# Optimization experiments

Measured on AMD Instinct MI355X. Metric: run time of the kernel, lower is better.

## Reference

```python
import jax, jax.numpy as jnp
import numpy as np

B, T, C = 4, 2048, 1024
N_HEADS = 16
HEAD_DIM = C // N_HEADS


def setup_inputs() -> dict:
    key = jax.random.key(0)
    k1, k2, k3, k4, k5 = jax.random.split(key, 5)
    x = jax.random.normal(k1, (B, T, C), dtype=jnp.float32)
    # torch Linear: y = x @ W.T + b; store W as [out, in]
    w_qkv = jax.random.normal(k2, (3 * C, C), dtype=jnp.float32) * (1.0 / np.sqrt(C))
    b_qkv = jax.random.normal(k3, (3 * C,), dtype=jnp.float32) * 0.01
    w_proj = jax.random.normal(k4, (C, C), dtype=jnp.float32) * (1.0 / np.sqrt(C))
    b_proj = jax.random.normal(k5, (C,), dtype=jnp.float32) * 0.01
    return {"x": x, "w_qkv": w_qkv, "b_qkv": b_qkv, "w_proj": w_proj, "b_proj": b_proj}


def reference(x, w_qkv, b_qkv, w_proj, b_proj):
    Bx, Tx, Cx = x.shape
    scale = 1.0 / np.sqrt(HEAD_DIM)
    qkv = x @ w_qkv.T + b_qkv                              # [B,T,3C]
    qkv = qkv.reshape(Bx, Tx, 3, N_HEADS, HEAD_DIM)
    qkv = jnp.transpose(qkv, (2, 0, 3, 1, 4))              # [3,B,H,T,D]
    q, k, v = qkv[0], qkv[1], qkv[2]
    att = jnp.einsum('bhqd,bhkd->bhqk', q, k) * scale      # [B,H,T,T]
    causal = jnp.tril(jnp.ones((Tx, Tx), dtype=bool))
    att = jnp.where(causal[None, None, :, :], att, -jnp.inf)
    att = jax.nn.softmax(att, axis=-1)
    # dropout p=0.0 (eval) -> identity
    out = jnp.einsum('bhqk,bhkd->bhqd', att, v)            # [B,H,T,D]
    out = jnp.transpose(out, (0, 2, 1, 3)).reshape(Bx, Tx, Cx)
    return out @ w_proj.T + b_proj
```

## Files before the change

kernel.cpp:

```cpp
#include <hip/hip_runtime.h>
#include <hip/hip_bf16.h>
#include <cstdint>

typedef __attribute__((ext_vector_type(8))) short bf16x8;
typedef __attribute__((ext_vector_type(4))) float f32x4;
typedef __attribute__((ext_vector_type(16))) float f32x16;

#define MFMA16(a, b, c) __builtin_amdgcn_mfma_f32_16x16x32_bf16(a, b, c, 0, 0, 0)
#define MFMA32(a, b, c) __builtin_amdgcn_mfma_f32_32x32x16_bf16(a, b, c, 0, 0, 0)

typedef __attribute__((address_space(1))) uint32_t as1_u32;
typedef __attribute__((address_space(3))) uint32_t as3_u32;
static __device__ __forceinline__ void gload16(const void* g, void* l) {
  __builtin_amdgcn_global_load_lds((as1_u32*)g, (as3_u32*)l, 16, 0, 0);
}

static __device__ __forceinline__ ushort f2b(float f) {
  union { float f; uint32_t u; } v; v.f = f;
  uint32_t u = v.u;
  uint32_t r = (u + 0x7FFFu + ((u >> 16) & 1u)) >> 16;
  return (ushort)r;
}

static __device__ __forceinline__ uint32_t cvtpk(float a, float b) {
  uint32_t r;
  asm("v_cvt_pk_bf16_f32 %0, %1, %2" : "=v"(r) : "v"(a), "v"(b));
  return r;
}
static __device__ __forceinline__ void plswap(uint32_t& a, uint32_t& b) {
  asm volatile("v_permlane32_swap_b32 %0, %1" : "+v"(a), "+v"(b));
}

#define QSCALE 0.1803368782f

#define LOFF(r, kc4) (((r) >> 1) * 64 + ((((((r) & 1) << 2) | (kc4)) ^ (((r) >> 1) & 7)) * 8))

#define N4_X  2097152
#define N4_WQ 786432
#define N4_WP 262144
__global__ void cvt_all(const float* __restrict__ x, const float* __restrict__ wq,
                        const float* __restrict__ wp, ushort* __restrict__ xb,
                        ushort* __restrict__ wqb, ushort* __restrict__ wpb) {
  int i = blockIdx.x * blockDim.x + threadIdx.x;
  const float* src; ushort* dst; int j;
  if (i < N4_X)            { src = x;  dst = xb;  j = i; }
  else if (i < N4_X + N4_WQ) { src = wq; dst = wqb; j = i - N4_X; }
  else                     { src = wp; dst = wpb; j = i - (N4_X + N4_WQ); }
  const float4 v = ((const float4*)src)[j];
  ushort4 o;
  o.x = f2b(v.x); o.y = f2b(v.y); o.z = f2b(v.z); o.w = f2b(v.w);
  ((ushort4*)dst)[j] = o;
}

template<int EPI>
__global__ __launch_bounds__(512, 2) void gemm_2ph(
    const ushort* __restrict__ A,
    const ushort* __restrict__ W,
    const float* __restrict__ bias,
    int M, int N, int K,
    ushort* __restrict__ q_ws, ushort* __restrict__ k_ws, ushort* __restrict__ v_ws,
    float* __restrict__ out) {
  __shared__ ushort As[2][2][64 * 64];
  __shared__ ushort Bs[2][2][2][64 * 64];
  const int tid = threadIdx.x;
  const int nbx = N >> 8;
  const int cpx = gridDim.x >> 3;
  const int wg = (blockIdx.x & 7) * cpx + (blockIdx.x >> 3);
  const int m0 = (wg / nbx) * 128, n0 = (wg % nbx) * 256;
  const int wid = tid >> 6, lane = tid & 63;
  const int wr = wid >> 2, wc = wid & 3;
  const int lr = lane & 15, lg = lane >> 4;
  const int prow = tid >> 3, pchk = tid & 7;
  const int lchk = pchk ^ (prow & 7);
  const int srow = prow * 2 + (lchk >> 2);
  const int skc = (lchk & 3) * 8;

  f32x4 acc[4][4] = {};
  const int nt = K >> 6;

#define STA(db_, kt_)                                                         \
  { const ushort* src = A + (size_t)(m0 + srow) * K + (kt_)*64 + skc;         \
    gload16(src, &As[db_][0][tid * 8]);                                       \
    gload16(src + 32, &As[db_][1][tid * 8]); }
#define STB(db_, half_, kt_)                                                  \
  { const ushort* src = W + (size_t)(n0 + (half_)*128 + srow) * K + (kt_)*64 + skc; \
    gload16(src, &Bs[db_][half_][0][tid * 8]);                                \
    gload16(src + 32, &Bs[db_][half_][1][tid * 8]); }

  STB(0, 0, 0); STB(0, 1, 0);
  STA(0, 0);
  STB(1, 0, 1); STB(1, 1, 1);
  asm volatile("s_waitcnt vmcnt(4)" ::: "memory");
  __builtin_amdgcn_s_barrier();

  const int bhalf = wc >> 1, brow = (wc & 1) * 64;
  for (int T = 0; T < nt; ++T) {
    const int db = T & 1;
    const ushort* Asub0 = &As[db][0][0];
    const ushort* Asub1 = &As[db][1][0];
    const ushort* Bsub0 = &Bs[db][bhalf][0][0];
    const ushort* Bsub1 = &Bs[db][bhalf][1][0];
    bf16x8 b[4][2];
    {
      bf16x8 a[2][2];
#pragma unroll
      for (int mm = 0; mm < 2; ++mm) {
        const int r = wr * 64 + mm * 16 + lr;
        a[mm][0] = *(const bf16x8*)&Asub0[LOFF(r, lg)];
        a[mm][1] = *(const bf16x8*)&Asub1[LOFF(r, lg)];
      }
#pragma unroll
      for (int nf = 0; nf < 4; ++nf) {
        const int r = brow + nf * 16 + lr;
        b[nf][0] = *(const bf16x8*)&Bsub0[LOFF(r, lg)];
        b[nf][1] = *(const bf16x8*)&Bsub1[LOFF(r, lg)];
      }
      if (T + 1 < nt) STA((T + 1) & 1, T + 1);
      __builtin_amdgcn_sched_barrier(0);
      __builtin_amdgcn_s_barrier();
      asm volatile("s_waitcnt lgkmcnt(0)" ::: "memory");
      __builtin_amdgcn_sched_barrier(0);
      __builtin_amdgcn_s_setprio(1);
#pragma unroll
      for (int kk = 0; kk < 2; ++kk)
#pragma unroll
        for (int mm = 0; mm < 2; ++mm)
#pragma unroll
          for (int nf = 0; nf < 4; ++nf)
            acc[mm][nf] = MFMA16(a[mm][kk], b[nf][kk], acc[mm][nf]);
      __builtin_amdgcn_s_setprio(0);
      __builtin_amdgcn_s_barrier();
    }
    {
      bf16x8 a[2][2];
#pragma unroll
      for (int mm = 0; mm < 2; ++mm) {
        const int r = wr * 64 + (2 + mm) * 16 + lr;
        a[mm][0] = *(const bf16x8*)&Asub0[LOFF(r, lg)];
        a[mm][1] = *(const bf16x8*)&Asub1[LOFF(r, lg)];
      }
      if (T + 2 < nt) { STB(db, 0, T + 2); STB(db, 1, T + 2); }
      __builtin_amdgcn_sched_barrier(0);
      __builtin_amdgcn_s_barrier();
      asm volatile("s_waitcnt lgkmcnt(0)" ::: "memory");
      __builtin_amdgcn_sched_barrier(0);
      __builtin_amdgcn_s_setprio(1);
#pragma unroll
      for (int kk = 0; kk < 2; ++kk)
#pragma unroll
        for (int mm = 0; mm < 2; ++mm)
#pragma unroll
          for (int nf = 0; nf < 4; ++nf)
            acc[2 + mm][nf] = MFMA16(a[mm][kk], b[nf][kk], acc[2 + mm][nf]);
      __builtin_amdgcn_s_setprio(0);
      if (T + 2 < nt)
        asm volatile("s_waitcnt vmcnt(4)" ::: "memory");
      else if (T + 1 < nt)
        asm volatile("s_waitcnt vmcnt(0)" ::: "memory");
      if (T + 1 < nt) __builtin_amdgcn_s_barrier();
    }
  }
#undef STA
#undef STB

#pragma unroll
  for (int mf = 0; mf < 4; ++mf) {
#pragma unroll
    for (int nf = 0; nf < 4; ++nf) {
      const int rowb = m0 + wr * 64 + mf * 16 + lg * 4;
      const int col = n0 + wc * 64 + nf * 16 + lr;
      float v[4];
#pragma unroll
      for (int i = 0; i < 4; ++i) v[i] = acc[mf][nf][i] + bias[col];
      if (EPI == 0) {
        const int sel = col >> 10;
        const int rem = col & 1023;
        const int h = rem >> 6, d = rem & 63;
        const int bb = rowb >> 11, t0 = rowb & 2047;
        if (sel == 2) {
          ushort4 st;
          st.x = f2b(v[0]); st.y = f2b(v[1]); st.z = f2b(v[2]); st.w = f2b(v[3]);
          *(ushort4*)&v_ws[((size_t)(bb * 16 + h) * 64 + d) * 2048 + t0] = st;
        } else if (sel == 0) {
#pragma unroll
          for (int i = 0; i < 4; ++i)
            q_ws[((size_t)(bb * 16 + h) * 2048 + t0 + i) * 64 + d] = f2b(v[i] * QSCALE);
        } else {
#pragma unroll
          for (int i = 0; i < 4; ++i)
            k_ws[((size_t)(bb * 16 + h) * 2048 + t0 + i) * 64 + d] = f2b(v[i]);
        }
      } else {
#pragma unroll
        for (int i = 0; i < 4; ++i)
          out[(size_t)(rowb + i) * N + col] = v[i];
      }
    }
  }
}

__global__ __launch_bounds__(256, 4) void attn_v6(
    const ushort* __restrict__ Q, const ushort* __restrict__ K,
    const ushort* __restrict__ VT, ushort* __restrict__ O ) {
  const int blk = blockIdx.x;
  const int s = 15 - (blk >> 6);
  const int bh = blk & 63;
  const int tid = threadIdx.x;
  const int w = tid >> 6, lane = tid & 63;
  const int l31 = lane & 31, l5 = lane >> 5;
  const int bb = bh >> 4, h = bh & 15;
  const size_t base = (size_t)bh * 2048 * 64;
  const ushort* Qb = Q + base;
  const ushort* Kb = K + base;
  const ushort* VTb = VT + base;

  __shared__ ushort Ks[2][64 * 64];
  __shared__ ushort Vs[2][64 * 64];
  __shared__ float l_lds[4][32];

#define STAGE(buf, kt_)                                              \
  do {                                                               \
    const ushort* Kt = Kb + (size_t)(kt_) * 64 * 64;                 \
    const ushort* Vt = VTb + (kt_) * 64;                             \
    _Pragma("unroll") for (int i_ = 0; i_ < 2; ++i_) {               \
      const int ch = i_ * 256 + tid;                                 \
      const int r = ch >> 3;                                         \
      const int csw = ((ch & 7) ^ (r & 7)) * 8;                      \
      gload16(&Kt[(size_t)r * 64 + csw], &Ks[buf][ch * 8]);          \
      gload16(&Vt[(size_t)r * 2048 + csw], &Vs[buf][ch * 8]);        \
    }                                                                \
  } while (0)

  const int q0w = s * 128 + w * 32;
  const int nt = 2 * s + 2;
  const int qlane = q0w + l31;

  bf16x8 qf[4];
#pragma unroll
  for (int dblk = 0; dblk < 4; ++dblk)
    qf[dblk] = *(const bf16x8*)&Qb[(size_t)qlane * 64 + dblk * 16 + l5 * 8];

  f32x16 o0 = {}, o1 = {};
  float lsum = 0.f;

  STAGE(0, 0);
  __syncthreads();

  for (int kt = 0; kt < nt; ++kt) {
    const int cur = kt & 1;
    if (kt + 1 < nt) STAGE(cur ^ 1, kt + 1);
    const int k0 = kt << 6;
    const ushort* Ksc = Ks[cur];
    const ushort* Vsc = Vs[cur];
#pragma unroll
    for (int kblk = 0; kblk < 2; ++kblk) {
      const int kbase = k0 + kblk * 32;
      if (kbase <= q0w + 31) {
        f32x16 st = {};
        __builtin_amdgcn_s_setprio(1);
#pragma unroll
        for (int dblk = 0; dblk < 4; ++dblk) {
          const int row = kblk * 32 + l31;
          bf16x8 ka = *(const bf16x8*)&Ksc[row * 64 + (((dblk * 2 + l5) ^ (row & 7)) * 8)];
          st = MFMA32(ka, qf[dblk], st);
        }
        __builtin_amdgcn_s_setprio(0);
        if (kbase + 31 > q0w) {
#pragma unroll
          for (int r = 0; r < 16; ++r) {
            const int kk = kbase + (r & 3) + 8 * (r >> 2) + 4 * l5;
            st[r] = (kk <= qlane) ? st[r] : -INFINITY;
          }
        }
        float p[16];
#pragma unroll
        for (int r = 0; r < 16; ++r) {
          p[r] = __builtin_amdgcn_exp2f(st[r]);
          lsum += p[r];
        }
#pragma unroll
        for (int sbl = 0; sbl < 2; ++sbl) {
          uint32_t P0 = cvtpk(p[8 * sbl + 0], p[8 * sbl + 1]);
          uint32_t P1 = cvtpk(p[8 * sbl + 2], p[8 * sbl + 3]);
          uint32_t P2 = cvtpk(p[8 * sbl + 4], p[8 * sbl + 5]);
          uint32_t P3 = cvtpk(p[8 * sbl + 6], p[8 * sbl + 7]);
          plswap(P0, P2);
          plswap(P1, P3);
          union { uint32_t u[4]; bf16x8 v; } pk;
          pk.u[0] = P0; pk.u[1] = P1; pk.u[2] = P2; pk.u[3] = P3;
          const int kchunk = kblk * 4 + sbl * 2 + l5;
          __builtin_amdgcn_s_setprio(1);
#pragma unroll
          for (int db2 = 0; db2 < 2; ++db2) {
            const int vrow = db2 * 32 + l31;
            bf16x8 vb = *(const bf16x8*)&Vsc[vrow * 64 + ((kchunk ^ (vrow & 7)) * 8)];
            if (db2 == 0) o0 = MFMA32(pk.v, vb, o0);
            else          o1 = MFMA32(pk.v, vb, o1);
          }
          __builtin_amdgcn_s_setprio(0);
        }
      }
    }
    __syncthreads();
  }

  const float lfull = lsum + __shfl_xor(lsum, 32);
  if (lane < 32) l_lds[w][lane] = 1.f / lfull;
#pragma unroll
  for (int r = 0; r < 16; ++r) {
    const int qoff = (r & 3) + 8 * (r >> 2) + 4 * l5;
    const float inv = l_lds[w][qoff];
    const int t = q0w + qoff;
    ushort* op = &O[(size_t)(bb * 2048 + t) * 1024 + h * 64 + l31];
    op[0] = f2b(o0[r] * inv);
    op[32] = f2b(o1[r] * inv);
  }
#undef STAGE
}

extern "C" void kernel_launch(void* const* d_in, const int* in_sizes, int n_in,
                              void* d_out, int out_size, void* d_ws, size_t ws_size,
                              hipStream_t stream) {
  const float* x = (const float*)d_in[0];
  const float* w_qkv = (const float*)d_in[1];
  const float* b_qkv = (const float*)d_in[2];
  const float* w_proj = (const float*)d_in[3];
  const float* b_proj = (const float*)d_in[4];
  float* out = (float*)d_out;

  char* ws = (char*)d_ws;
  const size_t SZ_X = (size_t)8192 * 1024 * 2;
  const size_t SZ_WQ = (size_t)3072 * 1024 * 2;
  const size_t SZ_WP = (size_t)1024 * 1024 * 2;
  ushort* xb = (ushort*)(ws);
  ushort* wqb = (ushort*)(ws + SZ_X);
  ushort* wpb = (ushort*)(ws + SZ_X + SZ_WQ);
  ushort* q_ws = (ushort*)(ws + SZ_X + SZ_WQ + SZ_WP);
  ushort* k_ws = q_ws + (size_t)8192 * 1024;
  ushort* v_ws = k_ws + (size_t)8192 * 1024;

  cvt_all<<<(N4_X + N4_WQ + N4_WP) / 256, 256, 0, stream>>>(
      x, w_qkv, w_proj, xb, wqb, wpb);

  gemm_2ph<0><<<768, 512, 0, stream>>>(
      xb, wqb, b_qkv, 8192, 3072, 1024, q_ws, k_ws, v_ws, nullptr);

  attn_v6<<<1024, 256, 0, stream>>>(q_ws, k_ws, v_ws, xb);

  gemm_2ph<1><<<256, 512, 0, stream>>>(
      xb, wpb, b_proj, 8192, 1024, 1024, nullptr, nullptr, nullptr, out);
}
```

Before: 156.7 us.

## Use 256x256 tiles for QKV GEMM with split A-phase pipeline

```diff
diff --git a/kernel.cpp b/kernel.cpp
--- a/kernel.cpp
+++ b/kernel.cpp
@@ -52,13 +52,149 @@
   ((ushort4*)dst)[j] = o;
 }
 
-template<int EPI>
-__global__ __launch_bounds__(512, 2) void gemm_2ph(
+__global__ __launch_bounds__(512, 2) void gemm_qkv256(
     const ushort* __restrict__ A,
     const ushort* __restrict__ W,
     const float* __restrict__ bias,
     int M, int N, int K,
-    ushort* __restrict__ q_ws, ushort* __restrict__ k_ws, ushort* __restrict__ v_ws,
+    ushort* __restrict__ q_ws, ushort* __restrict__ k_ws, ushort* __restrict__ v_ws) {
+  __shared__ ushort As[2][2][2][64 * 64];
+  __shared__ ushort Bs[2][2][2][64 * 64];
+  const int tid = threadIdx.x;
+  const int cpx = gridDim.x >> 3;
+  const int wg = (blockIdx.x & 7) * cpx + (blockIdx.x >> 3);
+  const int m0 = (wg / 12) * 256, n0 = (wg % 12) * 256;
+  const int wid = tid >> 6, lane = tid & 63;
+  const int wr = wid >> 2, wc = wid & 3;
+  const int lr = lane & 15, lg = lane >> 4;
+  const int bhalf = wc >> 1, brow = (wc & 1) * 64;
+  const int prow = tid >> 3, pchk = tid & 7;
+  const int lchk = pchk ^ (prow & 7);
+  const int srow = prow * 2 + (lchk >> 2);
+  const int skc = (lchk & 3) * 8;
+
+  f32x4 acc[8][4] = {};
+  const int nt = K >> 6;
+
+#define STA(db_, half_, kt_)                                                  \
+  { const ushort* src = A + (size_t)(m0 + (half_)*128 + srow) * K + (kt_)*64 + skc; \
+    gload16(src, &As[db_][half_][0][tid * 8]);                                \
+    gload16(src + 32, &As[db_][half_][1][tid * 8]); }
+#define STB(db_, half_, kt_)                                                  \
+  { const ushort* src = W + (size_t)(n0 + (half_)*128 + srow) * K + (kt_)*64 + skc; \
+    gload16(src, &Bs[db_][half_][0][tid * 8]);                                \
+    gload16(src + 32, &Bs[db_][half_][1][tid * 8]); }
+
+  STB(0, 0, 0); STB(0, 1, 0);
+  STA(0, 0, 0); STA(0, 1, 0);
+  STB(1, 0, 1); STB(1, 1, 1);
+  asm volatile("s_waitcnt vmcnt(4)" ::: "memory");
+  __builtin_amdgcn_s_barrier();
+
+  for (int T = 0; T < nt; ++T) {
+    const int db = T & 1;
+    const ushort* Ak0 = &As[db][wr][0][0];
+    const ushort* Ak1 = &As[db][wr][1][0];
+    const ushort* Bk0 = &Bs[db][bhalf][0][0];
+    const ushort* Bk1 = &Bs[db][bhalf][1][0];
+    bf16x8 b[4][2];
+    {
+      bf16x8 a[4][2];
+#pragma unroll
+      for (int mm = 0; mm < 4; ++mm) {
+        const int r = mm * 16 + lr;
+        a[mm][0] = *(const bf16x8*)&Ak0[LOFF(r, lg)];
+        a[mm][1] = *(const bf16x8*)&Ak1[LOFF(r, lg)];
+      }
+#pragma unroll
+      for (int nf = 0; nf < 4; ++nf) {
+        const int rr = brow + nf * 16 + lr;
+        b[nf][0] = *(const bf16x8*)&Bk0[LOFF(rr, lg)];
+        b[nf][1] = *(const bf16x8*)&Bk1[LOFF(rr, lg)];
+      }
+      if (T + 1 < nt) { STA(db ^ 1, 0, T + 1); STA(db ^ 1, 1, T + 1); }
+      __builtin_amdgcn_sched_barrier(0);
+      __builtin_amdgcn_s_barrier();
+      asm volatile("s_waitcnt lgkmcnt(0)" ::: "memory");
+      __builtin_amdgcn_sched_barrier(0);
+      __builtin_amdgcn_s_setprio(1);
+#pragma unroll
+      for (int kk = 0; kk < 2; ++kk)
+#pragma unroll
+        for (int mm = 0; mm < 4; ++mm)
+#pragma unroll
+          for (int nf = 0; nf < 4; ++nf)
+            acc[mm][nf] = MFMA16(a[mm][kk], b[nf][kk], acc[mm][nf]);
+      __builtin_amdgcn_s_setprio(0);
+      __builtin_amdgcn_s_barrier();
+    }
+    {
+      bf16x8 a[4][2];
+#pragma unroll
+      for (int mm = 0; mm < 4; ++mm) {
+        const int r = (4 + mm) * 16 + lr;
+        a[mm][0] = *(const bf16x8*)&Ak0[LOFF(r, lg)];
+        a[mm][1] = *(const bf16x8*)&Ak1[LOFF(r, lg)];
+      }
+      if (T + 2 < nt) { STB(db, 0, T + 2); STB(db, 1, T + 2); }
+      __builtin_amdgcn_sched_barrier(0);
+      __builtin_amdgcn_s_barrier();
+      asm volatile("s_waitcnt lgkmcnt(0)" ::: "memory");
+      __builtin_amdgcn_sched_barrier(0);
+      __builtin_amdgcn_s_setprio(1);
+#pragma unroll
+      for (int kk = 0; kk < 2; ++kk)
+#pragma unroll
+        for (int mm = 0; mm < 4; ++mm)
+#pragma unroll
+          for (int nf = 0; nf < 4; ++nf)
+            acc[4 + mm][nf] = MFMA16(a[mm][kk], b[nf][kk], acc[4 + mm][nf]);
+      __builtin_amdgcn_s_setprio(0);
+      if (T + 2 < nt)
+        asm volatile("s_waitcnt vmcnt(4)" ::: "memory");
+      else if (T + 1 < nt)
+        asm volatile("s_waitcnt vmcnt(0)" ::: "memory");
+      if (T + 1 < nt) __builtin_amdgcn_s_barrier();
+    }
+  }
+#undef STA
+#undef STB
+
+#pragma unroll
+  for (int mf = 0; mf < 8; ++mf) {
+#pragma unroll
+    for (int nf = 0; nf < 4; ++nf) {
+      const int rowb = m0 + wr * 128 + mf * 16 + lg * 4;
+      const int col = n0 + wc * 64 + nf * 16 + lr;
+      float v[4];
+#pragma unroll
+      for (int i = 0; i < 4; ++i) v[i] = acc[mf][nf][i] + bias[col];
+      const int sel = col >> 10;
+      const int rem = col & 1023;
+      const int h = rem >> 6, d = rem & 63;
+      const int bb = rowb >> 11, t0 = rowb & 2047;
+      if (sel == 2) {
+        ushort4 st;
+        st.x = f2b(v[0]); st.y = f2b(v[1]); st.z = f2b(v[2]); st.w = f2b(v[3]);
+        *(ushort4*)&v_ws[((size_t)(bb * 16 + h) * 64 + d) * 2048 + t0] = st;
+      } else if (sel == 0) {
+#pragma unroll
+        for (int i = 0; i < 4; ++i)
+          q_ws[((size_t)(bb * 16 + h) * 2048 + t0 + i) * 64 + d] = f2b(v[i] * QSCALE);
+      } else {
+#pragma unroll
+        for (int i = 0; i < 4; ++i)
+          k_ws[((size_t)(bb * 16 + h) * 2048 + t0 + i) * 64 + d] = f2b(v[i]);
+      }
+    }
+  }
+}
+
+__global__ __launch_bounds__(512, 2) void gemm_proj(
+    const ushort* __restrict__ A,
+    const ushort* __restrict__ W,
+    const float* __restrict__ bias,
+    int M, int N, int K,
     float* __restrict__ out) {
   __shared__ ushort As[2][2][64 * 64];
   __shared__ ushort Bs[2][2][2][64 * 64];
@@ -169,32 +305,9 @@
     for (int nf = 0; nf < 4; ++nf) {
       const int rowb = m0 + wr * 64 + mf * 16 + lg * 4;
       const int col = n0 + wc * 64 + nf * 16 + lr;
-      float v[4];
-#pragma unroll
-      for (int i = 0; i < 4; ++i) v[i] = acc[mf][nf][i] + bias[col];
-      if (EPI == 0) {
-        const int sel = col >> 10;
-        const int rem = col & 1023;
-        const int h = rem >> 6, d = rem & 63;
-        const int bb = rowb >> 11, t0 = rowb & 2047;
-        if (sel == 2) {
-          ushort4 st;
-          st.x = f2b(v[0]); st.y = f2b(v[1]); st.z = f2b(v[2]); st.w = f2b(v[3]);
-          *(ushort4*)&v_ws[((size_t)(bb * 16 + h) * 64 + d) * 2048 + t0] = st;
-        } else if (sel == 0) {
-#pragma unroll
-          for (int i = 0; i < 4; ++i)
-            q_ws[((size_t)(bb * 16 + h) * 2048 + t0 + i) * 64 + d] = f2b(v[i] * QSCALE);
-        } else {
-#pragma unroll
-          for (int i = 0; i < 4; ++i)
-            k_ws[((size_t)(bb * 16 + h) * 2048 + t0 + i) * 64 + d] = f2b(v[i]);
-        }
-      } else {
-#pragma unroll
-        for (int i = 0; i < 4; ++i)
-          out[(size_t)(rowb + i) * N + col] = v[i];
-      }
+#pragma unroll
+      for (int i = 0; i < 4; ++i)
+        out[(size_t)(rowb + i) * N + col] = acc[mf][nf][i] + bias[col];
     }
   }
 }
@@ -342,11 +455,11 @@
   cvt_all<<<(N4_X + N4_WQ + N4_WP) / 256, 256, 0, stream>>>(
       x, w_qkv, w_proj, xb, wqb, wpb);
 
-  gemm_2ph<0><<<768, 512, 0, stream>>>(
-      xb, wqb, b_qkv, 8192, 3072, 1024, q_ws, k_ws, v_ws, nullptr);
+  gemm_qkv256<<<384, 512, 0, stream>>>(
+      xb, wqb, b_qkv, 8192, 3072, 1024, q_ws, k_ws, v_ws);
 
   attn_v6<<<1024, 256, 0, stream>>>(q_ws, k_ws, v_ws, xb);
 
-  gemm_2ph<1><<<256, 512, 0, stream>>>(
-      xb, wpb, b_proj, 8192, 1024, 1024, nullptr, nullptr, nullptr, out);
-}
+  gemm_proj<<<256, 512, 0, stream>>>(
+      xb, wpb, b_proj, 8192, 1024, 1024, out);
+}
```

Result: no change. 157.4 us (+0.4%).
